# Optimization experiments

Hardware: AMD Instinct MI355X
Metric: run time of the kernel (lower is better)

Reference implementation:

```python
import jax, jax.numpy as jnp
import numpy as np

B, D, T, H, C = 65536, 1024, 16, 128, 10


def setup_inputs() -> dict:
    key = jax.random.key(0)
    k1, k2, k3, k4, k5, k6 = jax.random.split(key, 6)
    x = jax.random.normal(k1, (B, D), dtype=jnp.float32)
    task_id = jax.random.randint(k2, (B,), 0, T, dtype=jnp.int32)
    # per-task head params (torch nn.Linear init scale ~ 1/sqrt(fan_in))
    W1 = jax.random.normal(k3, (T, D, H), dtype=jnp.float32) / np.sqrt(D)
    b1 = jax.random.normal(k4, (T, H), dtype=jnp.float32) * 0.01
    W2 = jax.random.normal(k5, (T, H, C), dtype=jnp.float32) / np.sqrt(H)
    b2 = jax.random.normal(k6, (T, C), dtype=jnp.float32) * 0.01
    return {"x": x, "task_id": task_id, "W1": W1, "b1": b1, "W2": W2, "b2": b2}


def reference(x, task_id, W1, b1, W2, b2):
    # Dense dispatch: run every head on every sample as one big GEMM
    # (x @ [T*H] concatenated weights), then select each sample's task head.
    # Same math as the torch per-task mask/gather/scatter loop (eval mode,
    # dropout is identity).
    h = jax.nn.relu(jnp.einsum('bd,tdh->bth', x, W1) + b1)      # [B,T,H]
    logits_all = jnp.einsum('bth,thc->btc', h, W2) + b2          # [B,T,C]
    # gather the row for each sample's task_id
    logits = jnp.take_along_axis(
        logits_all, task_id[:, None, None].astype(jnp.int32), axis=1
    ).squeeze(1)                                                 # [B,C]
    return logits
```

## Files before the change

kernel.cpp:

```cpp
#include <hip/hip_runtime.h>
#include <hip/hip_bf16.h>

#define TASKS 16
#define DIM 1024
#define HID 128
#define NCLS 10
#define NB 65536
#define BM 128
#define NTILES (NB / BM + TASKS)

#define WS_TOT  4096
#define WS_RIDX 4160
#define WS_W1S  (WS_RIDX + NB)

typedef __attribute__((ext_vector_type(8))) short bf16x8;
typedef __attribute__((ext_vector_type(4))) float f32x4;
typedef __attribute__((ext_vector_type(2))) unsigned u32x2;

__device__ __forceinline__ unsigned short f2bf(float f) {
    union { __hip_bfloat16 h; unsigned short s; } u; u.h = __float2bfloat16(f); return u.s;
}

__device__ __forceinline__ void glds16(const void* gsrc, void* ldst) {
    __builtin_amdgcn_global_load_lds(
        (const __attribute__((address_space(1))) unsigned*)gsrc,
        (__attribute__((address_space(3))) unsigned*)ldst, 16, 0, 0);
}

__global__ __launch_bounds__(256) void k_pre(const int* __restrict__ tid_arr,
                                             const float* __restrict__ W1,
                                             const float* __restrict__ W2,
                                             int* __restrict__ ws) {
    const int blk = blockIdx.x, tid = threadIdx.x;
    if (blk < 256) {
        __shared__ int l[TASKS];
        if (tid < TASKS) l[tid] = 0;
        __syncthreads();
        atomicAdd(&l[tid_arr[blk * 256 + tid]], 1);
        __syncthreads();
        if (tid < TASKS) ws[blk * TASKS + tid] = l[tid];
    } else if (blk < 768) {
        const int idx = blk - 256;
        const int t = idx >> 5, kt = idx & 31;
        __shared__ float ld[32 * 132];
        const float* src = W1 + ((size_t)t * DIM + kt * 32) * HID;
        #pragma unroll
        for (int r = 0; r < 16; ++r) {
            const int fl = r * 256 + tid;
            ld[(fl >> 7) * 132 + (fl & 127)] = src[fl];
        }
        __syncthreads();
        char* dst = (char*)((short*)(ws + WS_W1S) + ((size_t)(t * 32 + kt) << 12));
        #pragma unroll
        for (int g = 0; g < 2; ++g) {
            const int p = tid * 32 + g * 16;
            const int kslot = p >> 11, col = (p >> 4) & 127;
            bf16x8 v;
            #pragma unroll
            for (int j = 0; j < 8; ++j)
                v[j] = (short)f2bf(ld[(kslot * 8 + j) * 132 + col]);
            *(bf16x8*)(dst + p) = v;
        }
    } else {
        const int t = blk - 768;
        short* W2t = (short*)(ws + WS_W1S) + ((size_t)TASKS * 32 * 4096);
        #pragma unroll
        for (int i = 0; i < 8; ++i) {
            const int o = i * 256 + tid, c = o >> 7, h = o & 127;
            const float v = (c < NCLS) ? W2[((size_t)t * HID + h) * NCLS + c] : 0.f;
            W2t[((size_t)t * 16 + c) * HID + h] = (short)f2bf(v);
        }
    }
}

__global__ __launch_bounds__(256) void k_scatter(const int* __restrict__ tid_arr,
                                                 int* __restrict__ ws) {
    __shared__ int part[256 * TASKS];
    __shared__ int sums[16 * TASKS];
    __shared__ int l[TASKS], offl[TASKS], prel[TASKS], totl[TASKS];
    const int b = blockIdx.x, tid = threadIdx.x;
    #pragma unroll
    for (int r = 0; r < 16; ++r) part[r * 256 + tid] = ws[r * 256 + tid];
    if (tid < TASKS) l[tid] = 0;
    __syncthreads();
    const int t = tid_arr[b * 256 + tid];
    const int rank = atomicAdd(&l[t], 1);
    {
        const int c = tid >> 4, tt = tid & 15;
        int s = 0;
        #pragma unroll
        for (int bb = 0; bb < 16; ++bb) s += part[(c * 16 + bb) * TASKS + tt];
        sums[c * TASKS + tt] = s;
    }
    __syncthreads();
    if (tid < TASKS) {
        const int cb = b >> 4;
        int pre = 0;
        for (int c = 0; c < cb; ++c) pre += sums[c * TASKS + tid];
        for (int bb = cb * 16; bb < b; ++bb) pre += part[bb * TASKS + tid];
        int tot = 0;
        #pragma unroll
        for (int c = 0; c < 16; ++c) tot += sums[c * TASKS + tid];
        prel[tid] = pre; totl[tid] = tot;
        if (b == 0) ws[WS_TOT + tid] = tot;
    }
    __syncthreads();
    if (tid == 0) {
        int ro = 0;
        for (int k = 0; k < TASKS; ++k) { offl[k] = ro; ro += totl[k]; }
    }
    __syncthreads();
    ws[WS_RIDX + offl[t] + prel[t] + rank] = b * 256 + tid;
}

__global__ __launch_bounds__(512, 4) void k_main(
    const float* __restrict__ x, const float* __restrict__ b1,
    const float* __restrict__ b2, const int* __restrict__ ws,
    float* __restrict__ out)
{
    __shared__ __align__(16) short smem[16384];
    __shared__ int ridx[BM];

    const int* tot = ws + WS_TOT;
    const int* rowIdx = ws + WS_RIDX;
    const short* W1s = (const short*)(ws + WS_W1S);
    const short* W2t = W1s + ((size_t)TASKS * 32 * 4096);

    const int w = (blockIdx.x & 7) * (NTILES / 8) + (blockIdx.x >> 3);

    int t = -1, m = 0, gstart = 0;
    {
        int accT = 0, accO = 0;
        for (int k = 0; k < TASKS; ++k) {
            const int c = tot[k], nt = (c + BM - 1) >> 7;
            if (t < 0 && w < accT + nt) {
                t = k; gstart = accO + (w - accT) * BM;
                m = c - (w - accT) * BM; if (m > BM) m = BM;
            }
            accT += nt; accO += c;
        }
    }
    if (t < 0) return;

    const int tid = threadIdx.x;
    if (tid < BM) ridx[tid] = rowIdx[gstart + (tid < m ? tid : m - 1)];
    __syncthreads();

    const int lane = tid & 63, wv = tid >> 6;
    const int lg = lane >> 4, lr = lane & 15;
    const int rh = wv & 1, cq = wv >> 1;
    const int wrow = rh * 64, wcol = cq * 32;

    const float* gpA[2];
    unsigned wbA[2];
    #pragma unroll
    for (int j = 0; j < 2; ++j) {
        const int row = wv * 16 + j * 8 + (lane >> 3);
        gpA[j] = x + ((size_t)ridx[row] << 10) + (lane & 7) * 4;
        wbA[j] = ((unsigned)((lane & 7) >> 1)) * 2048 + row * 16 + (lane & 1) * 8;
    }
    const char* w1sT = (const char*)W1s + ((size_t)t << 18);

    f32x4 a8[2];
    f32x4 acc[4][2] = {};

    auto LOADA = [&](int kt) {
        #pragma unroll
        for (int j = 0; j < 2; ++j) a8[j] = *(const f32x4*)(gpA[j] + kt * 32);
    };
    auto WRITEA = [&](int buf) {
        char* ab = (char*)smem + buf * 16384;
        #pragma unroll
        for (int j = 0; j < 2; ++j) {
            u32x2 pk;
            pk[0] = ((unsigned)f2bf(a8[j][1]) << 16) | (unsigned)f2bf(a8[j][0]);
            pk[1] = ((unsigned)f2bf(a8[j][3]) << 16) | (unsigned)f2bf(a8[j][2]);
            *(u32x2*)(ab + wbA[j]) = pk;
        }
    };
    auto ISSUEB = [&](int buf, int kt) {
        const char* src = w1sT + ((size_t)kt << 13) + wv * 1024 + lane * 16;
        char* dst = (char*)smem + buf * 16384 + 8192 + wv * 1024;
        glds16(src, dst);
    };
    auto COMPUTE = [&](int buf) {
        const char* ab = (const char*)smem + buf * 16384;
        const char* bb = ab + 8192;
        bf16x8 af[4], bfr[2];
        #pragma unroll
        for (int rf = 0; rf < 4; ++rf)
            af[rf] = *(const bf16x8*)(ab + lg * 2048 + (wrow + rf * 16 + lr) * 16);
        #pragma unroll
        for (int cf = 0; cf < 2; ++cf)
            bfr[cf] = *(const bf16x8*)(bb + lg * 2048 + (wcol + cf * 16 + lr) * 16);
        #pragma unroll
        for (int rf = 0; rf < 4; ++rf)
            #pragma unroll
            for (int cf = 0; cf < 2; ++cf)
                acc[rf][cf] = __builtin_amdgcn_mfma_f32_16x16x32_bf16(af[rf], bfr[cf], acc[rf][cf], 0, 0, 0);
    };

    LOADA(0);
    ISSUEB(0, 0);
    WRITEA(0);
    LOADA(1);
    asm volatile("s_waitcnt vmcnt(2) lgkmcnt(0)" ::: "memory");
    __builtin_amdgcn_s_barrier();
    __builtin_amdgcn_sched_barrier(0);

    #pragma unroll 2
    for (int kt = 0; kt < 32; ++kt) {
        const int buf = kt & 1;
        ISSUEB(buf ^ 1, kt + 1 < 32 ? kt + 1 : 31);
        WRITEA(buf ^ 1);
        LOADA(kt + 2 < 32 ? kt + 2 : 31);
        COMPUTE(buf);
        asm volatile("s_waitcnt vmcnt(2) lgkmcnt(0)" ::: "memory");
        __builtin_amdgcn_s_barrier();
        __builtin_amdgcn_sched_barrier(0);
    }
    __syncthreads();

    short* hl = smem;
    #pragma unroll
    for (int cf = 0; cf < 2; ++cf) {
        const int col = wcol + cf * 16 + lr;
        const float b1v = b1[t * HID + col];
        #pragma unroll
        for (int rf = 0; rf < 4; ++rf)
            #pragma unroll
            for (int q = 0; q < 4; ++q) {
                const int row = wrow + rf * 16 + lg * 4 + q;
                const float hv = fmaxf(acc[rf][cf][q] + b1v, 0.f);
                *(unsigned short*)((char*)hl + row * 256 +
                    (((col >> 3) ^ (row & 7)) << 4) + (col & 7) * 2) = f2bf(hv);
            }
    }
    __syncthreads();

    const int row2 = wv * 16 + lr;
    f32x4 acc2 = {};
    #pragma unroll
    for (int ks = 0; ks < 4; ++ks) {
        bf16x8 bvv = *(const bf16x8*)(W2t + (((size_t)t * 16 + lr) << 7) + ks * 32 + lg * 8);
        bf16x8 avv = *(const bf16x8*)((const char*)hl + row2 * 256 +
                         (((ks * 4 + lg) ^ (row2 & 7)) << 4));
        acc2 = __builtin_amdgcn_mfma_f32_16x16x32_bf16(avv, bvv, acc2, 0, 0, 0);
    }
    if (lr < NCLS) {
        const float b2v = b2[t * NCLS + lr];
        #pragma unroll
        for (int q = 0; q < 4; ++q) {
            const int row = wv * 16 + lg * 4 + q;
            if (row < m) out[(size_t)ridx[row] * NCLS + lr] = acc2[q] + b2v;
        }
    }
}

extern "C" void kernel_launch(void* const* d_in, const int* in_sizes, int n_in,
                              void* d_out, int out_size, void* d_ws, size_t ws_size,
                              hipStream_t stream) {
    (void)in_sizes; (void)n_in; (void)out_size; (void)ws_size;
    const float* x       = (const float*)d_in[0];
    const int*   task_id = (const int*)d_in[1];
    const float* W1      = (const float*)d_in[2];
    const float* b1      = (const float*)d_in[3];
    const float* W2      = (const float*)d_in[4];
    const float* b2      = (const float*)d_in[5];
    float* out = (float*)d_out;
    int* ws = (int*)d_ws;
    k_pre<<<784, 256, 0, stream>>>(task_id, W1, W2, ws);
    k_scatter<<<256, 256, 0, stream>>>(task_id, ws);
    k_main<<<NTILES, 512, 0, stream>>>(x, b1, b2, ws, out);
}
```

Baseline: 76.94 us.

## Double K-tile to 64, add XOR LDS swizzle and deeper A prefetch

The main GEMM loop now processes K in 64-wide tiles (16 iterations instead of 32), with LDS buffers doubled to 64KB total. W1 is repacked to match, with an XOR swizzle of column slots, and the A tiles are written with the same swizzle so LDS reads avoid bank conflicts. A three-deep register ring of prefetched x rows replaces the two-stage one, and the loop is fully unrolled. The aim is fewer barriers, better latency hiding and fewer LDS conflicts. The cost is more LDS and registers per block, which can lower occupancy under launch_bounds(512,4).

```diff
diff --git a/kernel.cpp b/kernel.cpp
--- a/kernel.cpp
+++ b/kernel.cpp
@@ -15,7 +15,6 @@
 
 typedef __attribute__((ext_vector_type(8))) short bf16x8;
 typedef __attribute__((ext_vector_type(4))) float f32x4;
-typedef __attribute__((ext_vector_type(2))) unsigned u32x2;
 
 __device__ __forceinline__ unsigned short f2bf(float f) {
     union { __hip_bfloat16 h; unsigned short s; } u; u.h = __float2bfloat16(f); return u.s;
@@ -39,22 +38,23 @@
         atomicAdd(&l[tid_arr[blk * 256 + tid]], 1);
         __syncthreads();
         if (tid < TASKS) ws[blk * TASKS + tid] = l[tid];
-    } else if (blk < 768) {
+    } else if (blk < 512) {
         const int idx = blk - 256;
-        const int t = idx >> 5, kt = idx & 31;
-        __shared__ float ld[32 * 132];
-        const float* src = W1 + ((size_t)t * DIM + kt * 32) * HID;
-        #pragma unroll
-        for (int r = 0; r < 16; ++r) {
+        const int t = idx >> 4, KT = idx & 15;
+        __shared__ float ld[64 * 132];
+        const float* src = W1 + ((size_t)t * DIM + KT * 64) * HID;
+        #pragma unroll
+        for (int r = 0; r < 32; ++r) {
             const int fl = r * 256 + tid;
             ld[(fl >> 7) * 132 + (fl & 127)] = src[fl];
         }
         __syncthreads();
-        char* dst = (char*)((short*)(ws + WS_W1S) + ((size_t)(t * 32 + kt) << 12));
-        #pragma unroll
-        for (int g = 0; g < 2; ++g) {
-            const int p = tid * 32 + g * 16;
-            const int kslot = p >> 11, col = (p >> 4) & 127;
+        char* dst = (char*)((short*)(ws + WS_W1S)) + ((size_t)(t * 16 + KT) << 14);
+        #pragma unroll
+        for (int g = 0; g < 4; ++g) {
+            const int p = tid * 64 + g * 16;
+            const int kslot = p >> 11, colslot = (p >> 4) & 127;
+            const int col = colslot ^ kslot;
             bf16x8 v;
             #pragma unroll
             for (int j = 0; j < 8; ++j)
@@ -62,7 +62,7 @@
             *(bf16x8*)(dst + p) = v;
         }
     } else {
-        const int t = blk - 768;
+        const int t = blk - 512;
         short* W2t = (short*)(ws + WS_W1S) + ((size_t)TASKS * 32 * 4096);
         #pragma unroll
         for (int i = 0; i < 8; ++i) {
@@ -118,7 +118,7 @@
     const float* __restrict__ b2, const int* __restrict__ ws,
     float* __restrict__ out)
 {
-    __shared__ __align__(16) short smem[16384];
+    __shared__ __align__(16) short smem[32768];
     __shared__ int ridx[BM];
 
     const int* tot = ws + WS_TOT;
@@ -151,71 +151,79 @@
     const int rh = wv & 1, cq = wv >> 1;
     const int wrow = rh * 64, wcol = cq * 32;
 
-    const float* gpA[2];
-    unsigned wbA[2];
-    #pragma unroll
-    for (int j = 0; j < 2; ++j) {
-        const int row = wv * 16 + j * 8 + (lane >> 3);
-        gpA[j] = x + ((size_t)ridx[row] << 10) + (lane & 7) * 4;
-        wbA[j] = ((unsigned)((lane & 7) >> 1)) * 2048 + row * 16 + (lane & 1) * 8;
-    }
+    const int arow0 = wv * 16 + (lane >> 3);
+    const int ks8 = lane & 7;
+    const float* gpA0 = x + ((size_t)ridx[arow0] << 10) + ks8 * 8;
+    const float* gpA1 = x + ((size_t)ridx[arow0 + 8] << 10) + ks8 * 8;
+    const unsigned wb0 = (unsigned)(ks8 * 2048 + ((arow0 ^ ks8) << 4));
+    const unsigned wb1 = (unsigned)(ks8 * 2048 + (((arow0 + 8) ^ ks8) << 4));
+
     const char* w1sT = (const char*)W1s + ((size_t)t << 18);
 
-    f32x4 a8[2];
+    f32x4 aR[3][4];
     f32x4 acc[4][2] = {};
 
-    auto LOADA = [&](int kt) {
-        #pragma unroll
-        for (int j = 0; j < 2; ++j) a8[j] = *(const f32x4*)(gpA[j] + kt * 32);
-    };
-    auto WRITEA = [&](int buf) {
-        char* ab = (char*)smem + buf * 16384;
-        #pragma unroll
-        for (int j = 0; j < 2; ++j) {
-            u32x2 pk;
-            pk[0] = ((unsigned)f2bf(a8[j][1]) << 16) | (unsigned)f2bf(a8[j][0]);
-            pk[1] = ((unsigned)f2bf(a8[j][3]) << 16) | (unsigned)f2bf(a8[j][2]);
-            *(u32x2*)(ab + wbA[j]) = pk;
-        }
-    };
-    auto ISSUEB = [&](int buf, int kt) {
-        const char* src = w1sT + ((size_t)kt << 13) + wv * 1024 + lane * 16;
-        char* dst = (char*)smem + buf * 16384 + 8192 + wv * 1024;
+    auto LOADA = [&](int s, int KT) {
+        aR[s][0] = *(const f32x4*)(gpA0 + KT * 64);
+        aR[s][1] = *(const f32x4*)(gpA0 + KT * 64 + 4);
+        aR[s][2] = *(const f32x4*)(gpA1 + KT * 64);
+        aR[s][3] = *(const f32x4*)(gpA1 + KT * 64 + 4);
+    };
+    auto WRITEA = [&](int buf, int s) {
+        char* ab = (char*)smem + buf * 32768;
+        bf16x8 p0, p1;
+        #pragma unroll
+        for (int e = 0; e < 4; ++e) { p0[e] = f2bf(aR[s][0][e]); p0[e+4] = f2bf(aR[s][1][e]); }
+        #pragma unroll
+        for (int e = 0; e < 4; ++e) { p1[e] = f2bf(aR[s][2][e]); p1[e+4] = f2bf(aR[s][3][e]); }
+        *(bf16x8*)(ab + wb0) = p0;
+        *(bf16x8*)(ab + wb1) = p1;
+    };
+    auto ISSUEB = [&](int buf, int KT) {
+        const char* src = w1sT + ((size_t)KT << 14) + wv * 2048 + lane * 16;
+        char* dst = (char*)smem + buf * 32768 + 16384 + wv * 2048;
         glds16(src, dst);
+        glds16(src + 1024, dst + 1024);
     };
     auto COMPUTE = [&](int buf) {
-        const char* ab = (const char*)smem + buf * 16384;
-        const char* bb = ab + 8192;
-        bf16x8 af[4], bfr[2];
-        #pragma unroll
-        for (int rf = 0; rf < 4; ++rf)
-            af[rf] = *(const bf16x8*)(ab + lg * 2048 + (wrow + rf * 16 + lr) * 16);
-        #pragma unroll
-        for (int cf = 0; cf < 2; ++cf)
-            bfr[cf] = *(const bf16x8*)(bb + lg * 2048 + (wcol + cf * 16 + lr) * 16);
-        #pragma unroll
-        for (int rf = 0; rf < 4; ++rf)
+        const char* ab = (const char*)smem + buf * 32768;
+        const char* bb = ab + 16384;
+        #pragma unroll
+        for (int ks = 0; ks < 2; ++ks) {
+            const int kslot = ks * 4 + lg;
+            const int koff = kslot * 2048;
+            bf16x8 af[4], bfr[2];
+            #pragma unroll
+            for (int rf = 0; rf < 4; ++rf)
+                af[rf] = *(const bf16x8*)(ab + koff + (((wrow + rf * 16 + lr) ^ kslot) << 4));
             #pragma unroll
             for (int cf = 0; cf < 2; ++cf)
-                acc[rf][cf] = __builtin_amdgcn_mfma_f32_16x16x32_bf16(af[rf], bfr[cf], acc[rf][cf], 0, 0, 0);
-    };
-
-    LOADA(0);
+                bfr[cf] = *(const bf16x8*)(bb + koff + (((wcol + cf * 16 + lr) ^ kslot) << 4));
+            #pragma unroll
+            for (int rf = 0; rf < 4; ++rf)
+                #pragma unroll
+                for (int cf = 0; cf < 2; ++cf)
+                    acc[rf][cf] = __builtin_amdgcn_mfma_f32_16x16x32_bf16(af[rf], bfr[cf], acc[rf][cf], 0, 0, 0);
+        }
+    };
+
+    LOADA(0, 0);
     ISSUEB(0, 0);
-    WRITEA(0);
-    LOADA(1);
-    asm volatile("s_waitcnt vmcnt(2) lgkmcnt(0)" ::: "memory");
+    LOADA(1, 1);
+    WRITEA(0, 0);
+    LOADA(2, 2);
+    asm volatile("s_waitcnt vmcnt(8) lgkmcnt(0)" ::: "memory");
     __builtin_amdgcn_s_barrier();
     __builtin_amdgcn_sched_barrier(0);
 
-    #pragma unroll 2
-    for (int kt = 0; kt < 32; ++kt) {
+    #pragma unroll
+    for (int kt = 0; kt < 16; ++kt) {
         const int buf = kt & 1;
-        ISSUEB(buf ^ 1, kt + 1 < 32 ? kt + 1 : 31);
-        WRITEA(buf ^ 1);
-        LOADA(kt + 2 < 32 ? kt + 2 : 31);
+        ISSUEB(buf ^ 1, kt + 1 < 16 ? kt + 1 : 15);
+        WRITEA(buf ^ 1, (kt + 1) % 3);
+        LOADA((kt + 3) % 3, kt + 3 < 16 ? kt + 3 : 15);
         COMPUTE(buf);
-        asm volatile("s_waitcnt vmcnt(2) lgkmcnt(0)" ::: "memory");
+        asm volatile("s_waitcnt vmcnt(4) lgkmcnt(0)" ::: "memory");
         __builtin_amdgcn_s_barrier();
         __builtin_amdgcn_sched_barrier(0);
     }
@@ -269,7 +277,7 @@
     const float* b2      = (const float*)d_in[5];
     float* out = (float*)d_out;
     int* ws = (int*)d_ws;
-    k_pre<<<784, 256, 0, stream>>>(task_id, W1, W2, ws);
+    k_pre<<<528, 256, 0, stream>>>(task_id, W1, W2, ws);
     k_scatter<<<256, 256, 0, stream>>>(task_id, ws);
     k_main<<<NTILES, 512, 0, stream>>>(x, b1, b2, ws, out);
 }
```

Result: slower. 79.30 us (+3.1%).

## Stream fp32 activations directly to LDS and triple-buffer the K loop

Applied to the files above, without the earlier changes.

Activation rows are now fetched with global_load_lds straight into shared memory as fp32, and converted to bf16 only when building MFMA fragments, which removes the register round trip and the separate LDS write stage. The pipeline goes from double to triple buffering, prefetching two k-tiles ahead with vmcnt-based waits. This costs far more LDS (72KB), which limits occupancy against the launch bound of 4 blocks, and it repeats the bf16 conversion in every wave that reads a fragment.

```diff
diff --git a/kernel.cpp b/kernel.cpp
--- a/kernel.cpp
+++ b/kernel.cpp
@@ -15,10 +15,15 @@
 
 typedef __attribute__((ext_vector_type(8))) short bf16x8;
 typedef __attribute__((ext_vector_type(4))) float f32x4;
-typedef __attribute__((ext_vector_type(2))) unsigned u32x2;
 
 __device__ __forceinline__ unsigned short f2bf(float f) {
     union { __hip_bfloat16 h; unsigned short s; } u; u.h = __float2bfloat16(f); return u.s;
+}
+__device__ __forceinline__ bf16x8 pack8(f32x4 a, f32x4 b) {
+    bf16x8 r;
+    r[0]=(short)f2bf(a[0]); r[1]=(short)f2bf(a[1]); r[2]=(short)f2bf(a[2]); r[3]=(short)f2bf(a[3]);
+    r[4]=(short)f2bf(b[0]); r[5]=(short)f2bf(b[1]); r[6]=(short)f2bf(b[2]); r[7]=(short)f2bf(b[3]);
+    return r;
 }
 
 __device__ __forceinline__ void glds16(const void* gsrc, void* ldst) {
@@ -118,7 +123,7 @@
     const float* __restrict__ b2, const int* __restrict__ ws,
     float* __restrict__ out)
 {
-    __shared__ __align__(16) short smem[16384];
+    __shared__ __align__(16) char smem[73728];
     __shared__ int ridx[BM];
 
     const int* tot = ws + WS_TOT;
@@ -148,80 +153,69 @@
 
     const int lane = tid & 63, wv = tid >> 6;
     const int lg = lane >> 4, lr = lane & 15;
-    const int rh = wv & 1, cq = wv >> 1;
-    const int wrow = rh * 64, wcol = cq * 32;
-
-    const float* gpA[2];
-    unsigned wbA[2];
-    #pragma unroll
-    for (int j = 0; j < 2; ++j) {
-        const int row = wv * 16 + j * 8 + (lane >> 3);
-        gpA[j] = x + ((size_t)ridx[row] << 10) + (lane & 7) * 4;
-        wbA[j] = ((unsigned)((lane & 7) >> 1)) * 2048 + row * 16 + (lane & 1) * 8;
-    }
+    const int wrow = (wv & 1) * 64, wcol = (wv >> 1) * 32;
+
+    const int ro = lane & 7, ch = lane >> 3;
+    const int rowA0 = wv * 16 + ro;
+    const int rowA1 = rowA0 + 8;
+    const float* srcA0 = x + ((size_t)ridx[rowA0] << 10) + ch * 4;
+    const float* srcA1 = x + ((size_t)ridx[rowA1] << 10) + ch * 4;
     const char* w1sT = (const char*)W1s + ((size_t)t << 18);
 
-    f32x4 a8[2];
     f32x4 acc[4][2] = {};
 
-    auto LOADA = [&](int kt) {
-        #pragma unroll
-        for (int j = 0; j < 2; ++j) a8[j] = *(const f32x4*)(gpA[j] + kt * 32);
+    auto ISSUE = [&](int bufIdx, int KT) {
+        char* bufb = smem + bufIdx * 24576;
+        glds16(srcA0 + KT * 32, bufb + (2 * wv) * 1024);
+        glds16(srcA1 + KT * 32, bufb + (2 * wv + 1) * 1024);
+        glds16(w1sT + ((size_t)KT << 13) + wv * 1024 + lane * 16,
+               bufb + 16384 + wv * 1024);
     };
-    auto WRITEA = [&](int buf) {
-        char* ab = (char*)smem + buf * 16384;
-        #pragma unroll
-        for (int j = 0; j < 2; ++j) {
-            u32x2 pk;
-            pk[0] = ((unsigned)f2bf(a8[j][1]) << 16) | (unsigned)f2bf(a8[j][0]);
-            pk[1] = ((unsigned)f2bf(a8[j][3]) << 16) | (unsigned)f2bf(a8[j][2]);
-            *(u32x2*)(ab + wbA[j]) = pk;
-        }
-    };
-    auto ISSUEB = [&](int buf, int kt) {
-        const char* src = w1sT + ((size_t)kt << 13) + wv * 1024 + lane * 16;
-        char* dst = (char*)smem + buf * 16384 + 8192 + wv * 1024;
-        glds16(src, dst);
-    };
-    auto COMPUTE = [&](int buf) {
-        const char* ab = (const char*)smem + buf * 16384;
-        const char* bb = ab + 8192;
+    auto COMPUTE = [&](int bufIdx) {
+        const char* ab = smem + bufIdx * 24576;
+        const char* bb = ab + 16384;
         bf16x8 af[4], bfr[2];
         #pragma unroll
-        for (int rf = 0; rf < 4; ++rf)
-            af[rf] = *(const bf16x8*)(ab + lg * 2048 + (wrow + rf * 16 + lr) * 16);
+        for (int rf = 0; rf < 4; ++rf) {
+            const int row = wrow + rf * 16 + lr;
+            const char* p = ab + ((row >> 3) << 10) + lg * 256 + ((row & 7) << 4);
+            f32x4 a0 = *(const f32x4*)p;
+            f32x4 a1 = *(const f32x4*)(p + 128);
+            af[rf] = pack8(a0, a1);
+        }
         #pragma unroll
         for (int cf = 0; cf < 2; ++cf)
-            bfr[cf] = *(const bf16x8*)(bb + lg * 2048 + (wcol + cf * 16 + lr) * 16);
+            bfr[cf] = *(const bf16x8*)(bb + lg * 2048 + ((wcol + cf * 16 + lr) << 4));
         #pragma unroll
         for (int rf = 0; rf < 4; ++rf)
             #pragma unroll
             for (int cf = 0; cf < 2; ++cf)
                 acc[rf][cf] = __builtin_amdgcn_mfma_f32_16x16x32_bf16(af[rf], bfr[cf], acc[rf][cf], 0, 0, 0);
     };
-
-    LOADA(0);
-    ISSUEB(0, 0);
-    WRITEA(0);
-    LOADA(1);
-    asm volatile("s_waitcnt vmcnt(2) lgkmcnt(0)" ::: "memory");
+    auto BODY = [&](int kt, int bc, int bn) {
+        ISSUE(bn, kt + 2 < 32 ? kt + 2 : 31);
+        COMPUTE(bc);
+        asm volatile("s_waitcnt vmcnt(3)" ::: "memory");
+        __builtin_amdgcn_s_barrier();
+        __builtin_amdgcn_sched_barrier(0);
+    };
+
+    ISSUE(0, 0);
+    ISSUE(1, 1);
+    asm volatile("s_waitcnt vmcnt(3)" ::: "memory");
     __builtin_amdgcn_s_barrier();
     __builtin_amdgcn_sched_barrier(0);
 
-    #pragma unroll 2
-    for (int kt = 0; kt < 32; ++kt) {
-        const int buf = kt & 1;
-        ISSUEB(buf ^ 1, kt + 1 < 32 ? kt + 1 : 31);
-        WRITEA(buf ^ 1);
-        LOADA(kt + 2 < 32 ? kt + 2 : 31);
-        COMPUTE(buf);
-        asm volatile("s_waitcnt vmcnt(2) lgkmcnt(0)" ::: "memory");
-        __builtin_amdgcn_s_barrier();
-        __builtin_amdgcn_sched_barrier(0);
-    }
-    __syncthreads();
-
-    short* hl = smem;
+    for (int k3 = 0; k3 < 30; k3 += 3) {
+        BODY(k3 + 0, 0, 2);
+        BODY(k3 + 1, 1, 0);
+        BODY(k3 + 2, 2, 1);
+    }
+    BODY(30, 0, 2);
+    BODY(31, 1, 0);
+    __syncthreads();
+
+    char* hl = smem;
     #pragma unroll
     for (int cf = 0; cf < 2; ++cf) {
         const int col = wcol + cf * 16 + lr;
@@ -232,7 +226,7 @@
             for (int q = 0; q < 4; ++q) {
                 const int row = wrow + rf * 16 + lg * 4 + q;
                 const float hv = fmaxf(acc[rf][cf][q] + b1v, 0.f);
-                *(unsigned short*)((char*)hl + row * 256 +
+                *(unsigned short*)(hl + row * 256 +
                     (((col >> 3) ^ (row & 7)) << 4) + (col & 7) * 2) = f2bf(hv);
             }
     }
@@ -243,8 +237,7 @@
     #pragma unroll
     for (int ks = 0; ks < 4; ++ks) {
         bf16x8 bvv = *(const bf16x8*)(W2t + (((size_t)t * 16 + lr) << 7) + ks * 32 + lg * 8);
-        bf16x8 avv = *(const bf16x8*)((const char*)hl + row2 * 256 +
-                         (((ks * 4 + lg) ^ (row2 & 7)) << 4));
+        bf16x8 avv = *(const bf16x8*)(hl + row2 * 256 + (((ks * 4 + lg) ^ (row2 & 7)) << 4));
         acc2 = __builtin_amdgcn_mfma_f32_16x16x32_bf16(avv, bvv, acc2, 0, 0, 0);
     }
     if (lr < NCLS) {
```

Measured after the change: 106.3 us. 1.38x slower.

## Replace two-pass prefix-sum scatter with global atomic bucketing into per-task arrays

Applied to the files above, without the earlier changes.

Drops the separate k_scatter kernel. Rows are now bucketed in the prep kernel by atomically reserving space in per-task index arrays sized NB each, with a memset zeroing the counters first. This removes one kernel launch and the serialized prefix-sum work. Row order within a task becomes nondeterministic, which should not change the output. Launch bounds for k_main are also raised from 4 to 6 waves per SIMD, which may limit registers and cause spills.

```diff
diff --git a/kernel.cpp b/kernel.cpp
--- a/kernel.cpp
+++ b/kernel.cpp
@@ -9,9 +9,8 @@
 #define BM 128
 #define NTILES (NB / BM + TASKS)
 
-#define WS_TOT  4096
-#define WS_RIDX 4160
-#define WS_W1S  (WS_RIDX + NB)
+#define WS_RIDX 64
+#define WS_W1S  (WS_RIDX + 16 * NB)
 
 typedef __attribute__((ext_vector_type(8))) short bf16x8;
 typedef __attribute__((ext_vector_type(4))) float f32x4;
@@ -27,18 +26,22 @@
         (__attribute__((address_space(3))) unsigned*)ldst, 16, 0, 0);
 }
 
-__global__ __launch_bounds__(256) void k_pre(const int* __restrict__ tid_arr,
-                                             const float* __restrict__ W1,
-                                             const float* __restrict__ W2,
-                                             int* __restrict__ ws) {
+__global__ __launch_bounds__(256) void k_prep(const int* __restrict__ tid_arr,
+                                              const float* __restrict__ W1,
+                                              const float* __restrict__ W2,
+                                              int* __restrict__ ws) {
     const int blk = blockIdx.x, tid = threadIdx.x;
     if (blk < 256) {
-        __shared__ int l[TASKS];
+        __shared__ int l[TASKS], base[TASKS];
         if (tid < TASKS) l[tid] = 0;
         __syncthreads();
-        atomicAdd(&l[tid_arr[blk * 256 + tid]], 1);
-        __syncthreads();
-        if (tid < TASKS) ws[blk * TASKS + tid] = l[tid];
+        const int i = blk * 256 + tid;
+        const int t = tid_arr[i];
+        const int rank = atomicAdd(&l[t], 1);
+        __syncthreads();
+        if (tid < TASKS && l[tid] > 0) base[tid] = atomicAdd(&ws[tid], l[tid]);
+        __syncthreads();
+        ws[WS_RIDX + t * NB + base[t] + rank] = i;
     } else if (blk < 768) {
         const int idx = blk - 256;
         const int t = idx >> 5, kt = idx & 31;
@@ -73,47 +76,7 @@
     }
 }
 
-__global__ __launch_bounds__(256) void k_scatter(const int* __restrict__ tid_arr,
-                                                 int* __restrict__ ws) {
-    __shared__ int part[256 * TASKS];
-    __shared__ int sums[16 * TASKS];
-    __shared__ int l[TASKS], offl[TASKS], prel[TASKS], totl[TASKS];
-    const int b = blockIdx.x, tid = threadIdx.x;
-    #pragma unroll
-    for (int r = 0; r < 16; ++r) part[r * 256 + tid] = ws[r * 256 + tid];
-    if (tid < TASKS) l[tid] = 0;
-    __syncthreads();
-    const int t = tid_arr[b * 256 + tid];
-    const int rank = atomicAdd(&l[t], 1);
-    {
-        const int c = tid >> 4, tt = tid & 15;
-        int s = 0;
-        #pragma unroll
-        for (int bb = 0; bb < 16; ++bb) s += part[(c * 16 + bb) * TASKS + tt];
-        sums[c * TASKS + tt] = s;
-    }
-    __syncthreads();
-    if (tid < TASKS) {
-        const int cb = b >> 4;
-        int pre = 0;
-        for (int c = 0; c < cb; ++c) pre += sums[c * TASKS + tid];
-        for (int bb = cb * 16; bb < b; ++bb) pre += part[bb * TASKS + tid];
-        int tot = 0;
-        #pragma unroll
-        for (int c = 0; c < 16; ++c) tot += sums[c * TASKS + tid];
-        prel[tid] = pre; totl[tid] = tot;
-        if (b == 0) ws[WS_TOT + tid] = tot;
-    }
-    __syncthreads();
-    if (tid == 0) {
-        int ro = 0;
-        for (int k = 0; k < TASKS; ++k) { offl[k] = ro; ro += totl[k]; }
-    }
-    __syncthreads();
-    ws[WS_RIDX + offl[t] + prel[t] + rank] = b * 256 + tid;
-}
-
-__global__ __launch_bounds__(512, 4) void k_main(
+__global__ __launch_bounds__(512, 6) void k_main(
     const float* __restrict__ x, const float* __restrict__ b1,
     const float* __restrict__ b2, const int* __restrict__ ws,
     float* __restrict__ out)
@@ -121,29 +84,32 @@
     __shared__ __align__(16) short smem[16384];
     __shared__ int ridx[BM];
 
-    const int* tot = ws + WS_TOT;
+    const int* tot = ws;
     const int* rowIdx = ws + WS_RIDX;
     const short* W1s = (const short*)(ws + WS_W1S);
     const short* W2t = W1s + ((size_t)TASKS * 32 * 4096);
 
     const int w = (blockIdx.x & 7) * (NTILES / 8) + (blockIdx.x >> 3);
 
-    int t = -1, m = 0, gstart = 0;
+    int t = -1, m = 0, tileInT = 0;
     {
-        int accT = 0, accO = 0;
+        int accT = 0;
         for (int k = 0; k < TASKS; ++k) {
             const int c = tot[k], nt = (c + BM - 1) >> 7;
             if (t < 0 && w < accT + nt) {
-                t = k; gstart = accO + (w - accT) * BM;
-                m = c - (w - accT) * BM; if (m > BM) m = BM;
+                t = k; tileInT = w - accT;
+                m = c - tileInT * BM; if (m > BM) m = BM;
             }
-            accT += nt; accO += c;
+            accT += nt;
         }
     }
     if (t < 0) return;
 
     const int tid = threadIdx.x;
-    if (tid < BM) ridx[tid] = rowIdx[gstart + (tid < m ? tid : m - 1)];
+    if (tid < BM) {
+        const int rr = tid < m ? tid : m - 1;
+        ridx[tid] = rowIdx[t * NB + tileInT * BM + rr];
+    }
     __syncthreads();
 
     const int lane = tid & 63, wv = tid >> 6;
@@ -269,7 +235,7 @@
     const float* b2      = (const float*)d_in[5];
     float* out = (float*)d_out;
     int* ws = (int*)d_ws;
-    k_pre<<<784, 256, 0, stream>>>(task_id, W1, W2, ws);
-    k_scatter<<<256, 256, 0, stream>>>(task_id, ws);
+    hipMemsetAsync(ws, 0, 64, stream);
+    k_prep<<<784, 256, 0, stream>>>(task_id, W1, W2, ws);
     k_main<<<NTILES, 512, 0, stream>>>(x, b1, b2, ws, out);
 }
```

New measurement: 78.13 us. No clear change (+1.6%).
